# Optimization experiments

Hardware: AMD Instinct MI355X
Metric: run time of the kernel (lower is better)

The kernel has to match this reference:

```python
import jax, jax.numpy as jnp
import numpy as np

IN_FEATURES = 3072
OUT_FEATURES = 12288
BLOCK = 32  # GGML Q8_0 block size


def setup_inputs() -> dict:
    key = jax.random.key(0)
    k_x, k_q, k_s, k_b = jax.random.split(key, 4)
    n_blocks = IN_FEATURES // BLOCK
    x = jax.random.normal(k_x, (4096, IN_FEATURES), dtype=jnp.float32)
    # int8-valued quants stored per Q8_0 block (kept as int32 carrier dtype)
    w_q = jax.random.randint(k_q, (OUT_FEATURES, n_blocks, BLOCK), -127, 128, dtype=jnp.int32)
    # one fp scale per 32-element block (small magnitude, like real d-values)
    scales = jax.random.uniform(k_s, (OUT_FEATURES, n_blocks, 1), dtype=jnp.float32) * 0.01
    bias = jax.random.normal(k_b, (OUT_FEATURES,), dtype=jnp.float32) * 0.02
    return {"x": x, "w_q": w_q, "scales": scales, "bias": bias}


def reference(x, w_q, scales, bias):
    # Block dequantization (GGML Q8_0: w = scale * int8_quant per 32-block),
    # materializing the full fp weight exactly as DequantingLinear.forward does,
    # then a standard F.linear: y = x @ W^T + b.
    out_f, n_blocks, block = w_q.shape
    W = (w_q.astype(x.dtype) * scales.astype(x.dtype)).reshape(out_f, n_blocks * block)
    return jnp.einsum("ti,oi->to", x, W) + bias.astype(x.dtype)
```

## Files before the change

### kernel.cpp

```cpp
#include <hip/hip_runtime.h>
#include <hip/hip_bf16.h>

typedef __bf16 bf16_t;
typedef __bf16 bf16x8 __attribute__((ext_vector_type(8)));
typedef float  f32x4  __attribute__((ext_vector_type(4)));
typedef int    i32x4  __attribute__((ext_vector_type(4)));
typedef signed char i8x16 __attribute__((ext_vector_type(16)));

#define M_DIM 4096
#define N_DIM 12288
#define K_DIM 3072
#define NBLK  96

#define BM 256
#define BN 256
#define BKB 128
#define THREADS 512
#define NT (K_DIM / BKB)

#define W8_OFF  ((size_t)0)
#define X8_OFF  ((size_t)N_DIM * K_DIM)
#define RO_OFF  (X8_OFF + (size_t)M_DIM * K_DIM)
#define ROI_OFF (RO_OFF + (size_t)N_DIM * 4)
#define SX_OFF  (ROI_OFF + (size_t)N_DIM * 4)
#define WS_NEED (SX_OFF + (size_t)M_DIM * 4)

#define WQB (N_DIM * K_DIM / 16 / 256)

#define BAR()   asm volatile("s_barrier" ::: "memory")
#define SBAR()  __builtin_amdgcn_sched_barrier(0)

__device__ __forceinline__ void gload_lds16(const void* g, void* l) {
    __builtin_amdgcn_global_load_lds(
        (const __attribute__((address_space(1))) unsigned int*)g,
        (__attribute__((address_space(3))) unsigned int*)l, 16, 0, 0);
}

__global__ __launch_bounds__(256) void romax_kernel(
    const float* __restrict__ scales, float* __restrict__ Ro,
    float* __restrict__ RoInv)
{
    int o = blockIdx.x * 256 + threadIdx.x;
    const float* p = scales + (size_t)o * NBLK;
    float mx = 1e-20f;
#pragma unroll
    for (int i = 0; i < 24; ++i) {
        f32x4 v = *(const f32x4*)(p + i * 4);
        mx = fmaxf(mx, fmaxf(fmaxf(v[0], v[1]), fmaxf(v[2], v[3])));
    }
    Ro[o] = mx;
    RoInv[o] = 1.f / mx;
}

__global__ __launch_bounds__(256) void xprep_kernel(
    const float* __restrict__ x, float* __restrict__ Sx,
    signed char* __restrict__ X8)
{
    const int row = blockIdx.x;
    const int tid = threadIdx.x;
    const float* p = x + (size_t)row * K_DIM;
    f32x4 v[3];
    float mx = 1e-20f;
#pragma unroll
    for (int i = 0; i < 3; ++i) {
        v[i] = *(const f32x4*)(p + i * 1024 + tid * 4);
        mx = fmaxf(mx, fmaxf(fmaxf(fabsf(v[i][0]), fabsf(v[i][1])),
                             fmaxf(fabsf(v[i][2]), fabsf(v[i][3]))));
    }
#pragma unroll
    for (int off = 32; off; off >>= 1) mx = fmaxf(mx, __shfl_xor(mx, off));
    __shared__ float red[4];
    if ((tid & 63) == 0) red[tid >> 6] = mx;
    __syncthreads();
    mx = fmaxf(fmaxf(red[0], red[1]), fmaxf(red[2], red[3]));
    if (tid == 0) Sx[row] = mx / 127.f;
    const float f = 127.f / mx;
    signed char* xo = X8 + (size_t)row * K_DIM;
#pragma unroll
    for (int i = 0; i < 3; ++i) {
        unsigned b0 = (unsigned)__float2int_rn(v[i][0] * f) & 0xffu;
        unsigned b1 = (unsigned)__float2int_rn(v[i][1] * f) & 0xffu;
        unsigned b2 = (unsigned)__float2int_rn(v[i][2] * f) & 0xffu;
        unsigned b3 = (unsigned)__float2int_rn(v[i][3] * f) & 0xffu;
        *(unsigned*)&xo[i * 1024 + tid * 4] = b0 | (b1 << 8) | (b2 << 16) | (b3 << 24);
    }
}

__global__ __launch_bounds__(256) void wquant_kernel(
    const int* __restrict__ wq, const float* __restrict__ scales,
    const float* __restrict__ RoInv, signed char* __restrict__ W8)
{
    unsigned c = blockIdx.x * 256u + threadIdx.x;
    unsigned o = c / 192u;
    unsigned j = c - o * 192u;
    float f = scales[o * NBLK + (j >> 1)] * RoInv[o];
    const int* gq = wq + (size_t)c * 16;
    i8x16 v;
#pragma unroll
    for (int i = 0; i < 4; ++i) {
        i32x4 q = *(const i32x4*)(gq + i * 4);
        v[i * 4 + 0] = (signed char)__float2int_rn((float)q[0] * f);
        v[i * 4 + 1] = (signed char)__float2int_rn((float)q[1] * f);
        v[i * 4 + 2] = (signed char)__float2int_rn((float)q[2] * f);
        v[i * 4 + 3] = (signed char)__float2int_rn((float)q[3] * f);
    }
    *(i8x16*)&W8[(size_t)c * 16] = v;
}

__global__ __launch_bounds__(THREADS, 2) void gemm_i8_kernel(
    const signed char* __restrict__ A8, const signed char* __restrict__ B8,
    const float* __restrict__ Ro, const float* __restrict__ Sx,
    const float* __restrict__ bias, float* __restrict__ out)
{
    __shared__ __align__(16) signed char sA8[2][BM * BKB];
    __shared__ __align__(16) signed char sB8[2][BN * BKB];

    const int tid  = threadIdx.x;
    const int bm   = blockIdx.x / (N_DIM / BN);
    const int bn   = blockIdx.x % (N_DIM / BN);
    const int row0 = bm * BM;
    const int col0 = bn * BN;

    const int lane = tid & 63;
    const int wid  = tid >> 6;
    const int wr   = (wid >> 2) * 128;
    const int wc   = (wid & 3) * 64;
    const int fr   = lane & 15;
    const int kq   = lane >> 4;

    const int rws = tid >> 3;
    const int c8s = (tid & 7) ^ (rws & 7);
    const signed char* srcA = A8 + (size_t)(row0 + rws) * K_DIM + c8s * 16;
    const signed char* srcB = B8 + (size_t)(col0 + rws) * K_DIM + c8s * 16;
    const int ldsU = (tid & ~63) * 16;

    auto stA = [&](int d, int uh, int tt) {
        const signed char* s = srcA + (size_t)tt * BKB + (size_t)uh * 128 * K_DIM;
        gload_lds16(s,                        &sA8[d][uh * 16384 + ldsU]);
        gload_lds16(s + (size_t)64 * K_DIM,   &sA8[d][uh * 16384 + 8192 + ldsU]);
    };
    auto stB = [&](int d, int uh, int tt) {
        const signed char* s = srcB + (size_t)tt * BKB + (size_t)uh * 128 * K_DIM;
        gload_lds16(s,                        &sB8[d][uh * 16384 + ldsU]);
        gload_lds16(s + (size_t)64 * K_DIM,   &sB8[d][uh * 16384 + 8192 + ldsU]);
    };

    i32x4 acc[8][4];
#pragma unroll
    for (int m = 0; m < 8; ++m)
#pragma unroll
        for (int n = 0; n < 4; ++n) acc[m][n] = (i32x4)0;

    auto rdA = [&](const signed char* pA, int rbase, i32x4 (&dst)[4][2]) {
#pragma unroll
        for (int m = 0; m < 4; ++m) {
            int row = rbase + m * 16 + fr;
#pragma unroll
            for (int ks = 0; ks < 2; ++ks) {
                int kc = ks * 4 + kq;
                dst[m][ks] = *(const i32x4*)(pA + row * BKB + ((kc ^ (row & 7)) << 4));
            }
        }
    };
    auto rdB = [&](const signed char* pB, int rbase, i32x4 (&dst)[2][2]) {
#pragma unroll
        for (int n = 0; n < 2; ++n) {
            int row = rbase + n * 16 + fr;
#pragma unroll
            for (int ks = 0; ks < 2; ++ks) {
                int kc = ks * 4 + kq;
                dst[n][ks] = *(const i32x4*)(pB + row * BKB + ((kc ^ (row & 7)) << 4));
            }
        }
    };
    auto mm = [&](i32x4 (&a)[4][2], i32x4 (&b)[2][2], int mo, int no) {
        __builtin_amdgcn_s_setprio(1);
#pragma unroll
        for (int m = 0; m < 4; ++m)
#pragma unroll
            for (int n = 0; n < 2; ++n)
#pragma unroll
                for (int ks = 0; ks < 2; ++ks)
                    acc[mo + m][no + n] = __builtin_amdgcn_mfma_i32_16x16x64_i8(
                        a[m][ks], b[n][ks], acc[mo + m][no + n], 0, 0, 0);
        __builtin_amdgcn_s_setprio(0);
    };

    i32x4 af0a[4][2], af1a[4][2], bg0a[2][2], bg1a[2][2];
    i32x4 af0b[4][2], af1b[4][2], bg0b[2][2], bg1b[2][2];

    stA(0, 0, 0); stA(0, 1, 0); stB(0, 0, 0); stB(0, 1, 0);
    stA(1, 0, 1); stA(1, 1, 1);
    asm volatile("s_waitcnt vmcnt(4)" ::: "memory");
    BAR();
    rdA(&sA8[0][0], wr, af0a); rdB(&sB8[0][0], wc, bg0a);

    auto ktile = [&](int cur, int t,
                     i32x4 (&AF0)[4][2], i32x4 (&AF1)[4][2],
                     i32x4 (&BG0)[2][2], i32x4 (&BG1)[2][2],
                     i32x4 (&AF0n)[4][2], i32x4 (&BG0n)[2][2]) {
        const signed char* pA  = &sA8[cur][0];
        const signed char* pB  = &sB8[cur][0];
        const signed char* pAn = &sA8[cur ^ 1][0];
        const signed char* pBn = &sB8[cur ^ 1][0];
        int t1 = t + 1; if (t1 >= NT) t1 -= NT;
        int t2 = t + 2; if (t2 >= NT) t2 -= NT;

        rdA(pA, wr + 64, AF1);
        stB(cur ^ 1, 0, t1);
        SBAR();
        mm(AF0, BG0, 0, 0);

        rdB(pB, wc + 32, BG1);
        stB(cur ^ 1, 1, t1);
        SBAR();
        mm(AF1, BG0, 4, 0);
        BAR();

        stA(cur, 0, t2);
        stA(cur, 1, t2);
        SBAR();
        mm(AF1, BG1, 4, 2);
        SBAR();
        asm volatile("s_waitcnt vmcnt(4)" ::: "memory");
        BAR();

        rdA(pAn, wr, AF0n); rdB(pBn, wc, BG0n);
        SBAR();
        mm(AF0, BG1, 0, 2);
    };

    for (int it = 0; it < NT / 2; ++it) {
        ktile(0, it * 2,     af0a, af1a, bg0a, bg1a, af0b, bg0b);
        ktile(1, it * 2 + 1, af0b, af1b, bg0b, bg1b, af0a, bg0a);
    }

    const int crow = (lane >> 4) << 2;
    const int ccol = lane & 15;
    float ro[4], bb[4];
#pragma unroll
    for (int n = 0; n < 4; ++n) {
        int col = col0 + wc + n * 16 + ccol;
        ro[n] = Ro[col];
        bb[n] = bias[col];
    }
#pragma unroll
    for (int m = 0; m < 8; ++m) {
#pragma unroll
        for (int j = 0; j < 4; ++j) {
            int row = row0 + wr + m * 16 + crow + j;
            float sx = Sx[row];
            size_t base = (size_t)row * N_DIM + col0 + wc + ccol;
#pragma unroll
            for (int n = 0; n < 4; ++n)
                out[base + n * 16] = (float)acc[m][n][j] * ro[n] * sx + bb[n];
        }
    }
}

#define FBM 128
#define FBN 128
#define FBK 64
#define FTHREADS 256
__global__ __launch_bounds__(FTHREADS) void dq_gemm_fused_kernel(
    const float* __restrict__ x, const int* __restrict__ wq,
    const float* __restrict__ scales, const float* __restrict__ bias,
    float* __restrict__ out)
{
    __shared__ bf16_t fA[FBM * FBK];
    __shared__ bf16_t fB[FBN * FBK];

    const int tid  = threadIdx.x;
    const int bm   = blockIdx.x / (N_DIM / FBN);
    const int bn   = blockIdx.x % (N_DIM / FBN);
    const int row0 = bm * FBM;
    const int col0 = bn * FBN;
    const int lane = tid & 63;
    const int wid  = tid >> 6;
    const int wr   = (wid >> 1) * 64;
    const int wc   = (wid & 1) * 64;
    const int fr   = lane & 15;
    const int fk   = (lane >> 4) << 3;

    f32x4 acc[4][4];
#pragma unroll
    for (int m = 0; m < 4; ++m)
#pragma unroll
        for (int n = 0; n < 4; ++n) acc[m][n] = (f32x4)0.f;

    for (int kt = 0; kt < K_DIM / FBK; ++kt) {
        const int kb = kt * FBK;
#pragma unroll
        for (int c = 0; c < 4; ++c) {
            int i  = c * FTHREADS + tid;
            int r  = i >> 3;
            int k0 = (i & 7) << 3;
            const float* gp = x + (size_t)(row0 + r) * K_DIM + kb + k0;
            f32x4 f0 = *(const f32x4*)gp;
            f32x4 f1 = *(const f32x4*)(gp + 4);
            bf16x8 v;
            v[0] = (bf16_t)f0[0]; v[1] = (bf16_t)f0[1];
            v[2] = (bf16_t)f0[2]; v[3] = (bf16_t)f0[3];
            v[4] = (bf16_t)f1[0]; v[5] = (bf16_t)f1[1];
            v[6] = (bf16_t)f1[2]; v[7] = (bf16_t)f1[3];
            *(bf16x8*)&fA[r * FBK + (k0 ^ ((r & 7) << 3))] = v;
        }
#pragma unroll
        for (int c = 0; c < 4; ++c) {
            int i  = c * FTHREADS + tid;
            int r  = i >> 3;
            int k0 = (i & 7) << 3;
            int o  = col0 + r;
            const int* gq = wq + (size_t)o * K_DIM + kb + k0;
            i32x4 q0 = *(const i32x4*)gq;
            i32x4 q1 = *(const i32x4*)(gq + 4);
            float s = scales[o * NBLK + ((kb + k0) >> 5)];
            bf16x8 v;
            v[0] = (bf16_t)((float)q0[0] * s); v[1] = (bf16_t)((float)q0[1] * s);
            v[2] = (bf16_t)((float)q0[2] * s); v[3] = (bf16_t)((float)q0[3] * s);
            v[4] = (bf16_t)((float)q1[0] * s); v[5] = (bf16_t)((float)q1[1] * s);
            v[6] = (bf16_t)((float)q1[2] * s); v[7] = (bf16_t)((float)q1[3] * s);
            *(bf16x8*)&fB[r * FBK + (k0 ^ ((r & 7) << 3))] = v;
        }
        __syncthreads();
#pragma unroll
        for (int ks = 0; ks < 2; ++ks) {
            bf16x8 af[4], bg[4];
#pragma unroll
            for (int m = 0; m < 4; ++m) {
                int r = wr + m * 16 + fr;
                af[m] = *(const bf16x8*)&fA[r * FBK + ((ks * 32 + fk) ^ ((r & 7) << 3))];
            }
#pragma unroll
            for (int n = 0; n < 4; ++n) {
                int r = wc + n * 16 + fr;
                bg[n] = *(const bf16x8*)&fB[r * FBK + ((ks * 32 + fk) ^ ((r & 7) << 3))];
            }
#pragma unroll
            for (int m = 0; m < 4; ++m)
#pragma unroll
                for (int n = 0; n < 4; ++n)
                    acc[m][n] = __builtin_amdgcn_mfma_f32_16x16x32_bf16(
                        af[m], bg[n], acc[m][n], 0, 0, 0);
        }
        __syncthreads();
    }

    const int crow = (lane >> 4) << 2;
    const int ccol = lane & 15;
#pragma unroll
    for (int m = 0; m < 4; ++m) {
#pragma unroll
        for (int n = 0; n < 4; ++n) {
            int col = col0 + wc + n * 16 + ccol;
            float b = bias[col];
#pragma unroll
            for (int j = 0; j < 4; ++j) {
                int row = row0 + wr + m * 16 + crow + j;
                out[(size_t)row * N_DIM + col] = acc[m][n][j] + b;
            }
        }
    }
}

extern "C" void kernel_launch(void* const* d_in, const int* in_sizes, int n_in,
                              void* d_out, int out_size, void* d_ws, size_t ws_size,
                              hipStream_t stream) {
    const float* x      = (const float*)d_in[0];
    const int*   wq     = (const int*)d_in[1];
    const float* scales = (const float*)d_in[2];
    const float* bias   = (const float*)d_in[3];
    float*       out    = (float*)d_out;

    if (ws_size >= WS_NEED) {
        signed char* W8    = (signed char*)d_ws + W8_OFF;
        signed char* X8    = (signed char*)d_ws + X8_OFF;
        float*       Ro    = (float*)((char*)d_ws + RO_OFF);
        float*       RoInv = (float*)((char*)d_ws + ROI_OFF);
        float*       Sx    = (float*)((char*)d_ws + SX_OFF);

        romax_kernel<<<dim3(N_DIM / 256), dim3(256), 0, stream>>>(scales, Ro, RoInv);
        xprep_kernel<<<dim3(M_DIM), dim3(256), 0, stream>>>(x, Sx, X8);
        wquant_kernel<<<dim3(WQB), dim3(256), 0, stream>>>(wq, scales, RoInv, W8);
        gemm_i8_kernel<<<dim3((M_DIM / BM) * (N_DIM / BN)), dim3(THREADS), 0, stream>>>(
            X8, W8, Ro, Sx, bias, out);
    } else {
        dq_gemm_fused_kernel<<<dim3((M_DIM / FBM) * (N_DIM / FBN)), dim3(FTHREADS), 0, stream>>>(
            x, wq, scales, bias, out);
    }
}
```

Before: 208.6 us.

## Use 4 waves with 128x128 per-wave tiles in int8 GEMM

Halves the GEMM block from 8 to 4 waves, giving each wave a 128x128 output tile (8x8 MFMA accumulators) instead of 128x64. Each wave then reuses its A and B LDS fragments across more MFMAs, which cuts LDS reads per MFMA, and the global-to-LDS load loops are rebalanced for 256 threads. In exchange the accumulator register count doubles, occupancy drops to one block per CU, and each thread issues twice as many async loads, so latency hiding may suffer.

```diff
diff --git a/kernel.cpp b/kernel.cpp
--- a/kernel.cpp
+++ b/kernel.cpp
@@ -15,7 +15,7 @@
 #define BM 256
 #define BN 256
 #define BKB 128
-#define THREADS 512
+#define THREADS 256
 #define NT (K_DIM / BKB)
 
 #define W8_OFF  ((size_t)0)
@@ -107,7 +107,7 @@
     *(i8x16*)&W8[(size_t)c * 16] = v;
 }
 
-__global__ __launch_bounds__(THREADS, 2) void gemm_i8_kernel(
+__global__ __launch_bounds__(THREADS, 1) void gemm_i8w_kernel(
     const signed char* __restrict__ A8, const signed char* __restrict__ B8,
     const float* __restrict__ Ro, const float* __restrict__ Sx,
     const float* __restrict__ bias, float* __restrict__ out)
@@ -123,8 +123,8 @@
 
     const int lane = tid & 63;
     const int wid  = tid >> 6;
-    const int wr   = (wid >> 2) * 128;
-    const int wc   = (wid & 3) * 64;
+    const int wr   = (wid >> 1) * 128;
+    const int wc   = (wid & 1) * 128;
     const int fr   = lane & 15;
     const int kq   = lane >> 4;
 
@@ -134,51 +134,42 @@
     const signed char* srcB = B8 + (size_t)(col0 + rws) * K_DIM + c8s * 16;
     const int ldsU = (tid & ~63) * 16;
 
-    auto stA = [&](int d, int uh, int tt) {
-        const signed char* s = srcA + (size_t)tt * BKB + (size_t)uh * 128 * K_DIM;
-        gload_lds16(s,                        &sA8[d][uh * 16384 + ldsU]);
-        gload_lds16(s + (size_t)64 * K_DIM,   &sA8[d][uh * 16384 + 8192 + ldsU]);
-    };
-    auto stB = [&](int d, int uh, int tt) {
-        const signed char* s = srcB + (size_t)tt * BKB + (size_t)uh * 128 * K_DIM;
-        gload_lds16(s,                        &sB8[d][uh * 16384 + ldsU]);
-        gload_lds16(s + (size_t)64 * K_DIM,   &sB8[d][uh * 16384 + 8192 + ldsU]);
-    };
-
-    i32x4 acc[8][4];
+    auto stA = [&](int d, int tt) {
+#pragma unroll
+        for (int j = 0; j < 8; ++j)
+            gload_lds16(srcA + (size_t)tt * BKB + (size_t)(j * 32) * K_DIM,
+                        &sA8[d][j * 4096 + ldsU]);
+    };
+    auto stB = [&](int d, int h, int tt) {
+#pragma unroll
+        for (int j = 0; j < 4; ++j)
+            gload_lds16(srcB + (size_t)tt * BKB + (size_t)((h * 4 + j) * 32) * K_DIM,
+                        &sB8[d][(h * 4 + j) * 4096 + ldsU]);
+    };
+
+    i32x4 acc[8][8];
 #pragma unroll
     for (int m = 0; m < 8; ++m)
 #pragma unroll
-        for (int n = 0; n < 4; ++n) acc[m][n] = (i32x4)0;
-
-    auto rdA = [&](const signed char* pA, int rbase, i32x4 (&dst)[4][2]) {
+        for (int n = 0; n < 8; ++n) acc[m][n] = (i32x4)0;
+
+    auto rdF = [&](const signed char* p, int rbase, i32x4 (&dst)[4][2]) {
 #pragma unroll
         for (int m = 0; m < 4; ++m) {
             int row = rbase + m * 16 + fr;
 #pragma unroll
             for (int ks = 0; ks < 2; ++ks) {
                 int kc = ks * 4 + kq;
-                dst[m][ks] = *(const i32x4*)(pA + row * BKB + ((kc ^ (row & 7)) << 4));
+                dst[m][ks] = *(const i32x4*)(p + row * BKB + ((kc ^ (row & 7)) << 4));
             }
         }
     };
-    auto rdB = [&](const signed char* pB, int rbase, i32x4 (&dst)[2][2]) {
-#pragma unroll
-        for (int n = 0; n < 2; ++n) {
-            int row = rbase + n * 16 + fr;
-#pragma unroll
-            for (int ks = 0; ks < 2; ++ks) {
-                int kc = ks * 4 + kq;
-                dst[n][ks] = *(const i32x4*)(pB + row * BKB + ((kc ^ (row & 7)) << 4));
-            }
-        }
-    };
-    auto mm = [&](i32x4 (&a)[4][2], i32x4 (&b)[2][2], int mo, int no) {
+    auto mm = [&](i32x4 (&a)[4][2], i32x4 (&b)[4][2], int mo, int no) {
         __builtin_amdgcn_s_setprio(1);
 #pragma unroll
         for (int m = 0; m < 4; ++m)
 #pragma unroll
-            for (int n = 0; n < 2; ++n)
+            for (int n = 0; n < 4; ++n)
 #pragma unroll
                 for (int ks = 0; ks < 2; ++ks)
                     acc[mo + m][no + n] = __builtin_amdgcn_mfma_i32_16x16x64_i8(
@@ -186,19 +177,19 @@
         __builtin_amdgcn_s_setprio(0);
     };
 
-    i32x4 af0a[4][2], af1a[4][2], bg0a[2][2], bg1a[2][2];
-    i32x4 af0b[4][2], af1b[4][2], bg0b[2][2], bg1b[2][2];
-
-    stA(0, 0, 0); stA(0, 1, 0); stB(0, 0, 0); stB(0, 1, 0);
-    stA(1, 0, 1); stA(1, 1, 1);
-    asm volatile("s_waitcnt vmcnt(4)" ::: "memory");
+    i32x4 af0a[4][2], bg0a[4][2];
+    i32x4 af0b[4][2], bg0b[4][2];
+
+    stA(0, 0);
+    stB(0, 0, 0); stB(0, 1, 0);
+    stA(1, 1);
+    asm volatile("s_waitcnt vmcnt(8)" ::: "memory");
     BAR();
-    rdA(&sA8[0][0], wr, af0a); rdB(&sB8[0][0], wc, bg0a);
+    rdF(&sA8[0][0], wr, af0a); rdF(&sB8[0][0], wc, bg0a);
 
     auto ktile = [&](int cur, int t,
-                     i32x4 (&AF0)[4][2], i32x4 (&AF1)[4][2],
-                     i32x4 (&BG0)[2][2], i32x4 (&BG1)[2][2],
-                     i32x4 (&AF0n)[4][2], i32x4 (&BG0n)[2][2]) {
+                     i32x4 (&AF0)[4][2], i32x4 (&BG0)[4][2],
+                     i32x4 (&AF0n)[4][2], i32x4 (&BG0n)[4][2]) {
         const signed char* pA  = &sA8[cur][0];
         const signed char* pB  = &sB8[cur][0];
         const signed char* pAn = &sA8[cur ^ 1][0];
@@ -206,40 +197,41 @@
         int t1 = t + 1; if (t1 >= NT) t1 -= NT;
         int t2 = t + 2; if (t2 >= NT) t2 -= NT;
 
-        rdA(pA, wr + 64, AF1);
+        i32x4 AF1[4][2], BG1[4][2];
+
+        rdF(pA, wr + 64, AF1);
         stB(cur ^ 1, 0, t1);
         SBAR();
         mm(AF0, BG0, 0, 0);
 
-        rdB(pB, wc + 32, BG1);
+        rdF(pB, wc + 64, BG1);
         stB(cur ^ 1, 1, t1);
         SBAR();
         mm(AF1, BG0, 4, 0);
         BAR();
 
-        stA(cur, 0, t2);
-        stA(cur, 1, t2);
-        SBAR();
-        mm(AF1, BG1, 4, 2);
-        SBAR();
-        asm volatile("s_waitcnt vmcnt(4)" ::: "memory");
+        stA(cur, t2);
+        SBAR();
+        mm(AF1, BG1, 4, 4);
+        SBAR();
+        asm volatile("s_waitcnt vmcnt(8)" ::: "memory");
         BAR();
 
-        rdA(pAn, wr, AF0n); rdB(pBn, wc, BG0n);
-        SBAR();
-        mm(AF0, BG1, 0, 2);
+        rdF(pAn, wr, AF0n); rdF(pBn, wc, BG0n);
+        SBAR();
+        mm(AF0, BG1, 0, 4);
     };
 
     for (int it = 0; it < NT / 2; ++it) {
-        ktile(0, it * 2,     af0a, af1a, bg0a, bg1a, af0b, bg0b);
-        ktile(1, it * 2 + 1, af0b, af1b, bg0b, bg1b, af0a, bg0a);
+        ktile(0, it * 2,     af0a, bg0a, af0b, bg0b);
+        ktile(1, it * 2 + 1, af0b, bg0b, af0a, bg0a);
     }
 
     const int crow = (lane >> 4) << 2;
     const int ccol = lane & 15;
-    float ro[4], bb[4];
-#pragma unroll
-    for (int n = 0; n < 4; ++n) {
+    float ro[8], bb[8];
+#pragma unroll
+    for (int n = 0; n < 8; ++n) {
         int col = col0 + wc + n * 16 + ccol;
         ro[n] = Ro[col];
         bb[n] = bias[col];
@@ -252,7 +244,7 @@
             float sx = Sx[row];
             size_t base = (size_t)row * N_DIM + col0 + wc + ccol;
 #pragma unroll
-            for (int n = 0; n < 4; ++n)
+            for (int n = 0; n < 8; ++n)
                 out[base + n * 16] = (float)acc[m][n][j] * ro[n] * sx + bb[n];
         }
     }
@@ -382,7 +374,7 @@
         romax_kernel<<<dim3(N_DIM / 256), dim3(256), 0, stream>>>(scales, Ro, RoInv);
         xprep_kernel<<<dim3(M_DIM), dim3(256), 0, stream>>>(x, Sx, X8);
         wquant_kernel<<<dim3(WQB), dim3(256), 0, stream>>>(wq, scales, RoInv, W8);
-        gemm_i8_kernel<<<dim3((M_DIM / BM) * (N_DIM / BN)), dim3(THREADS), 0, stream>>>(
+        gemm_i8w_kernel<<<dim3((M_DIM / BM) * (N_DIM / BN)), dim3(THREADS), 0, stream>>>(
             X8, W8, Ro, Sx, bias, out);
     } else {
         dq_gemm_fused_kernel<<<dim3((M_DIM / FBM) * (N_DIM / FBN)), dim3(FTHREADS), 0, stream>>>(
```

Measured after the change: 480.6 us. 2.3x slower.
